# Kernel tuning notes

Hardware: AMD Instinct MI355X
Metric: run time of the kernel (lower is better)

The kernel has to match this reference:

```python
import jax, jax.numpy as jnp
import numpy as np

B, N, F, D, H, L, K = 128, 128, 13, 256, 8, 8, 10
FF = 2 * D  # FFN / hidden width
HEAD = D // H


def setup_inputs() -> dict:
    key = jax.random.key(0)
    ks = iter(jax.random.split(key, 64))
    def nrm(shape, scale=0.02):
        return jax.random.normal(next(ks), shape, dtype=jnp.float32) * scale
    return {
        "input_features": jax.random.normal(next(ks), (B, N, F), dtype=jnp.float32),
        "input_points": jax.random.normal(next(ks), (B, N, 2), dtype=jnp.float32),
        "input_mask": jnp.ones((B, N, 1), dtype=jnp.float32),
        "input_time": jax.random.uniform(next(ks), (B, 1), dtype=jnp.float32),
        # get_encoding: Dense(2D, gelu) -> Dense(D, gelu)
        "enc_w1": nrm((F, FF)), "enc_b1": jnp.zeros((FF,), jnp.float32),
        "enc_w2": nrm((FF, D)), "enc_b2": jnp.zeros((D,), jnp.float32),
        # FourierProjection MLP (no bias, swish)
        "four_w1": nrm((D, FF)), "four_w2": nrm((FF, D)),
        # FiLM time projection (no bias)
        "time_w": nrm((D, FF)),
        # local KNN MLPs: round 0 input 2*F, round 1 input 2*D
        "loc1_w1": nrm((2 * F, FF)), "loc1_b1": jnp.zeros((FF,), jnp.float32),
        "loc1_w2": nrm((FF, D)), "loc1_b2": jnp.zeros((D,), jnp.float32),
        "loc2_w1": nrm((2 * D, FF)), "loc2_b1": jnp.zeros((FF,), jnp.float32),
        "loc2_w2": nrm((FF, D)), "loc2_b2": jnp.zeros((D,), jnp.float32),
        # transformer encoder layers, stacked over L
        "qkv_w": nrm((L, D, 3 * D)), "qkv_b": jnp.zeros((L, 3 * D), jnp.float32),
        "out_w": nrm((L, D, D)), "out_b": jnp.zeros((L, D), jnp.float32),
        "ln1_g": jnp.ones((L, D), jnp.float32), "ln1_b": jnp.zeros((L, D), jnp.float32),
        "ff1_w": nrm((L, D, FF)), "ff1_b": jnp.zeros((L, FF), jnp.float32),
        "ff2_w": nrm((L, FF, D)), "ff2_b": jnp.zeros((L, D), jnp.float32),
        "gamma": jnp.full((L, D), 1e-5, dtype=jnp.float32),
        "ln2_g": jnp.ones((L, D), jnp.float32), "ln2_b": jnp.zeros((L, D), jnp.float32),
    }


def _ln(x, g, b, eps=1e-5):
    m = jnp.mean(x, axis=-1, keepdims=True)
    v = jnp.var(x, axis=-1, keepdims=True)
    return (x - m) * jax.lax.rsqrt(v + eps) * g + b


def _fourier(t, w1, w2):
    # t: (B,1) -> (B,D)
    half = D // 2
    emb = np.log(10000.0) / (half - 1)
    freq = jnp.exp(-emb * jnp.arange(half, dtype=jnp.float32))
    angle = t * freq[None, :] * 1000.0  # (B, half)
    e = jnp.concatenate([jnp.sin(angle), jnp.cos(angle)], axis=-1)
    e = jax.nn.silu(e @ w1)
    return jax.nn.silu(e @ w2)


def _get_neighbors(points, feats, w1, b1, w2, b2):
    # points: (B,N,P), feats: (B,N,C) -> (B,N,D)
    r = jnp.sum(points * points, axis=-1)  # (B,N)
    d = r[:, :, None] - 2.0 * jnp.einsum('bnp,bmp->bnm', points, points) + r[:, None, :]
    _, idx = jax.lax.top_k(-d, K + 1)
    idx = idx[:, :, 1:]  # drop self, (B,N,K)
    knn = jax.vmap(lambda f, i: f[i])(feats, idx)  # (B,N,K,C)
    center = jnp.broadcast_to(feats[:, :, None, :], knn.shape)
    local = jnp.concatenate([knn - center, center], axis=-1)  # (B,N,K,2C)
    local = jax.nn.gelu(local @ w1 + b1)
    local = jax.nn.gelu(local @ w2 + b2)
    return jnp.mean(local, axis=2)


def _mha(x, mask, wqkv, bqkv, wo, bo):
    Bx, Nx, _ = x.shape
    qkv = x @ wqkv + bqkv
    q, k, v = jnp.split(qkv, 3, axis=-1)
    def heads(t):
        return t.reshape(Bx, Nx, H, HEAD).transpose(0, 2, 1, 3)
    q, k, v = heads(q), heads(k), heads(v)
    scores = jnp.einsum('bhqd,bhkd->bhqk', q, k) * (1.0 / np.sqrt(HEAD))
    keep = mask[:, None, None, :, 0] > 0  # (B,1,1,N)
    scores = jnp.where(keep, scores, -1e9)
    a = jax.nn.softmax(scores, axis=-1)
    o = jnp.einsum('bhqk,bhkd->bhqd', a, v).transpose(0, 2, 1, 3).reshape(Bx, Nx, D)
    return o @ wo + bo


def _pet(input_features, input_points, input_mask, input_time,
         enc_w1, enc_b1, enc_w2, enc_b2, four_w1, four_w2, time_w,
         loc1_w1, loc1_b1, loc1_w2, loc1_b2, loc2_w1, loc2_b1, loc2_w2, loc2_b2,
         qkv_w, qkv_b, out_w, out_b, ln1_g, ln1_b, ff1_w, ff1_b, ff2_w, ff2_b,
         gamma, ln2_g, ln2_b):
    # feature encoding (RandomDrop is identity at eval / feature_drop=0)
    enc = jax.nn.gelu(input_features @ enc_w1 + enc_b1)
    enc = jax.nn.gelu(enc @ enc_w2 + enc_b2)  # (B,N,D)
    # FiLM time conditioning
    t = _fourier(input_time, four_w1, four_w2)  # (B,D)
    t = t[:, None, :] * input_mask  # (B,N,D)
    scale, shift = jnp.split(t @ time_w, 2, axis=-1)
    enc = enc * (1.0 + scale) + shift
    # local KNN aggregation
    coord_shift = 999.0 * (1.0 - input_mask)  # (B,N,1)
    points = input_points[:, :, :2]
    lf = _get_neighbors(coord_shift + points, input_features, loc1_w1, loc1_b1, loc1_w2, loc1_b2)
    lf = _get_neighbors(coord_shift + lf, lf, loc2_w1, loc2_b1, loc2_w2, loc2_b2)
    enc = enc + lf
    skip = enc
    x = enc
    for i in range(L):
        res = x
        a = _mha(x, input_mask, qkv_w[i], qkv_b[i], out_w[i], out_b[i])
        x = _ln(res + a, ln1_g[i], ln1_b[i])
        res = x
        h = jax.nn.gelu(x @ ff1_w[i] + ff1_b[i])
        h = h @ ff2_w[i] + ff2_b[i]
        h = h * gamma[i] * input_mask  # LayerScale with mask
        x = _ln(res + h, ln2_g[i], ln2_b[i])
    return x + skip


def reference(input_features, input_points, input_mask, input_time,
              enc_w1, enc_b1, enc_w2, enc_b2, four_w1, four_w2, time_w,
              loc1_w1, loc1_b1, loc1_w2, loc1_b2, loc2_w1, loc2_b1, loc2_w2, loc2_b2,
              qkv_w, qkv_b, out_w, out_b, ln1_g, ln1_b, ff1_w, ff1_b, ff2_w, ff2_b,
              gamma, ln2_g, ln2_b):
    return _pet(input_features, input_points, input_mask, input_time,
                enc_w1, enc_b1, enc_w2, enc_b2, four_w1, four_w2, time_w,
                loc1_w1, loc1_b1, loc1_w2, loc1_b2, loc2_w1, loc2_b1, loc2_w2, loc2_b2,
                qkv_w, qkv_b, out_w, out_b, ln1_g, ln1_b, ff1_w, ff1_b, ff2_w, ff2_b,
                gamma, ln2_g, ln2_b)
```

## Files before the change

### kernel.cpp

```cpp
#include <hip/hip_runtime.h>
#include <hip/hip_bf16.h>
#include <cmath>

#define DEV_INLINE __device__ __forceinline__

constexpr int Bn = 128;
constexpr int Nn = 128;
constexpr int Fn = 13;
constexpr int Dn = 256;
constexpr int Ln = 8;
constexpr int Kn = 10;
constexpr int FFn = 512;
constexpr int Tn = Bn * Nn;
constexpr int Rn = Tn * Kn;

typedef __attribute__((ext_vector_type(4))) float f32x4;
typedef __attribute__((ext_vector_type(8))) short bf16x8;
typedef unsigned short us;

__device__ float g_x[Tn * Dn];
__device__ float g_skip[Tn * Dn];
__device__ float g_big[Tn * Dn];
__device__ float g_dm[Tn * Nn];
__device__ float g_u[Bn * FFn];
__device__ float g_r[Tn];
__device__ float g_pqbias[2048];
__device__ int   g_idx[Rn];
__device__ us g_bigb[Tn * 768];
__device__ us g_xb[Tn * Dn];
__device__ us g_attb[Tn * Dn];
__device__ us g_lf1b[Tn * Dn];
__device__ us g_pq[Tn * 1024];
__device__ us g_h2b[Rn * Dn];
__device__ us g_feat16[Tn * 32];
constexpr int OFF_ENC1 = 0;
constexpr int OFF_ENC2 = OFF_ENC1 + 512 * 32;
constexpr int OFF_W2A  = OFF_ENC2 + 256 * 512;
constexpr int OFF_W2B  = OFF_W2A + 256 * 512;
constexpr int OFF_PQ1  = OFF_W2B + 256 * 512;
constexpr int OFF_PQ2  = OFF_PQ1 + 1024 * 32;
constexpr int OFF_QKV  = OFF_PQ2 + 1024 * 256;
constexpr int OFF_OUT  = OFF_QKV + 8 * 768 * 256;
constexpr int OFF_FF1  = OFF_OUT + 8 * 256 * 256;
constexpr int OFF_FF2  = OFF_FF1 + 8 * 512 * 256;
constexpr int WT_TOTAL = OFF_FF2 + 8 * 256 * 512;
__device__ us g_wt[WT_TOTAL];

DEV_INLINE float gelu_f(float x) {
    float x2 = x * x;
    float m = x * fmaf(x2, -0.07135537f, -1.59576912f);
    float t = __expf(m);
    return x * __builtin_amdgcn_rcpf(1.f + t);
}
DEV_INLINE us f2b(float x) {
    __hip_bfloat16 h = __float2bfloat16(x);
    return *(us*)&h;
}
DEV_INLINE float blo(unsigned u) { return __uint_as_float(u << 16); }
DEV_INLINE float bhi(unsigned u) { return __uint_as_float(u & 0xFFFF0000u); }
DEV_INLINE unsigned pk2(float a, float b) {
    float2 f; f.x = a; f.y = b;
    __hip_bfloat162 h = __float22bfloat162_rn(f);
    return *(unsigned*)&h;
}

#define GLOAD16(gp, lp)                                                            \
    __builtin_amdgcn_global_load_lds(                                              \
        (const __attribute__((address_space(1))) unsigned int*)(gp),               \
        (__attribute__((address_space(3))) unsigned int*)(lp), 16, 0, 0)

constexpr int U0 = 0;
constexpr int U1 = U0 + 2;
constexpr int U2 = U1 + 16;
constexpr int U3 = U2 + 16;
constexpr int U4 = U3 + 16;
constexpr int U5 = U4 + 192;
constexpr int U6 = U5 + 64;
constexpr int U7 = U6 + 128;
constexpr int U8 = U7 + 128;
constexpr int U9 = U8 + 128;
constexpr int U10 = U9 + 128;
constexpr int U11 = U10 + 256;
constexpr int U12 = U11 + 128;
constexpr int UPN = U12 + 128;

DEV_INLINE void prep_seg(const float* __restrict__ src, us* __restrict__ dst,
                         int Kreal, int Kpad, int Nd, long sstride, long dstride,
                         int gx, int gy, int lb, int tid, float* tile) {
    int z = lb / (gx * gy);
    int rem = lb - z * gx * gy;
    int by = rem / gx, bx = rem - by * gx;
    const float* s = src + (size_t)z * sstride;
    us* d = dst + (size_t)z * dstride;
    int cn = tid & 31, rk = tid >> 5;
    int kbase = by * 32, nbase = bx * 32;
#pragma unroll
    for (int p = 0; p < 4; p++) {
        int k = kbase + p * 8 + rk;
        float v = (k < Kreal) ? s[(size_t)k * Nd + nbase + cn] : 0.f;
        tile[(p * 8 + rk) * 33 + cn] = v;
    }
    __syncthreads();
#pragma unroll
    for (int p = 0; p < 4; p++) {
        int nl = p * 8 + rk;
        d[(size_t)(nbase + nl) * Kpad + kbase + cn] = f2b(tile[cn * 33 + nl]);
    }
    __syncthreads();
}

DEV_INLINE void prepPQ_seg(const float* __restrict__ w1, const float* __restrict__ b1,
                           us* __restrict__ dst, float* __restrict__ bdst,
                           int Kreal, int Kpad, int n, int tid) {
    for (int k = tid; k < Kpad; k += 256) {
        float v;
        if (n < 512) v = (k < Kreal) ? w1[(size_t)k * 512 + n] : 0.f;
        else {
            int m = n - 512;
            v = (k < Kreal) ? (w1[(size_t)(Kreal + k) * 512 + m] - w1[(size_t)k * 512 + m]) : 0.f;
        }
        dst[(size_t)n * Kpad + k] = f2b(v);
    }
    if (tid == 0) bdst[n] = (n < 512) ? 0.f : b1[n - 512];
}

__global__ __launch_bounds__(256) void k_uprep(
    const float* __restrict__ enc_w1, const float* __restrict__ enc_w2,
    const float* __restrict__ l1w2, const float* __restrict__ l2w2,
    const float* __restrict__ qkv_w, const float* __restrict__ out_w,
    const float* __restrict__ ff1w, const float* __restrict__ ff2w,
    const float* __restrict__ l1w1, const float* __restrict__ l1b1,
    const float* __restrict__ l2w1, const float* __restrict__ l2b1,
    const float* __restrict__ feat, const float* __restrict__ tin,
    const float* __restrict__ four_w1, const float* __restrict__ four_w2,
    const float* __restrict__ time_w, const float* __restrict__ pts,
    const float* __restrict__ mask,
    us* __restrict__ wt, float* __restrict__ pqbias, us* __restrict__ fp,
    float* __restrict__ u, int* __restrict__ idx) {
    __shared__ float shmem[1056];
    int b = blockIdx.x, tid = threadIdx.x;
    if (b < U1) {
#pragma unroll 1
        for (int i = 0; i < 8; i++)
            prep_seg(enc_w1, wt + OFF_ENC1, 13, 32, 512, 0, 0, 16, 1, (b - U0) * 8 + i, tid, shmem);
    } else if (b < U2) {
#pragma unroll 1
        for (int i = 0; i < 8; i++)
            prep_seg(enc_w2, wt + OFF_ENC2, 512, 512, 256, 0, 0, 8, 16, (b - U1) * 8 + i, tid, shmem);
    } else if (b < U3) {
#pragma unroll 1
        for (int i = 0; i < 8; i++)
            prep_seg(l1w2, wt + OFF_W2A, 512, 512, 256, 0, 0, 8, 16, (b - U2) * 8 + i, tid, shmem);
    } else if (b < U4) {
#pragma unroll 1
        for (int i = 0; i < 8; i++)
            prep_seg(l2w2, wt + OFF_W2B, 512, 512, 256, 0, 0, 8, 16, (b - U3) * 8 + i, tid, shmem);
    } else if (b < U5) {
#pragma unroll 1
        for (int i = 0; i < 8; i++)
            prep_seg(qkv_w, wt + OFF_QKV, 256, 256, 768, 256 * 768, 768 * 256, 24, 8, (b - U4) * 8 + i, tid, shmem);
    } else if (b < U6) {
#pragma unroll 1
        for (int i = 0; i < 8; i++)
            prep_seg(out_w, wt + OFF_OUT, 256, 256, 256, 256 * 256, 256 * 256, 8, 8, (b - U5) * 8 + i, tid, shmem);
    } else if (b < U7) {
#pragma unroll 1
        for (int i = 0; i < 8; i++)
            prep_seg(ff1w, wt + OFF_FF1, 256, 256, 512, 256 * 512, 512 * 256, 16, 8, (b - U6) * 8 + i, tid, shmem);
    } else if (b < U8) {
#pragma unroll 1
        for (int i = 0; i < 8; i++)
            prep_seg(ff2w, wt + OFF_FF2, 512, 512, 256, 512 * 256, 256 * 512, 8, 16, (b - U7) * 8 + i, tid, shmem);
    } else if (b < U9) {
#pragma unroll 1
        for (int i = 0; i < 8; i++)
            prepPQ_seg(l1w1, l1b1, wt + OFF_PQ1, pqbias, 13, 32, (b - U8) * 8 + i, tid);
    } else if (b < U10) {
#pragma unroll 1
        for (int i = 0; i < 8; i++)
            prepPQ_seg(l2w1, l2b1, wt + OFF_PQ2, pqbias + 1024, 256, 256, (b - U9) * 8 + i, tid);
    } else if (b < U11) {
#pragma unroll 1
        for (int i = 0; i < 8; i++) {
            int gid = ((b - U10) * 8 + i) * 256 + tid;
            int t = gid >> 5, c = gid & 31;
            fp[gid] = (c < Fn) ? f2b(feat[(size_t)t * Fn + c]) : (us)0;
        }
    } else if (b < U12) {
        float* e = shmem; float* e1 = shmem + 256; float* t2 = shmem + 768;
        int bb = b - U11;
        float tv = tin[bb];
        if (tid < 128) {
            const float emb = 0.07252236513366287f;
            float fr = expf(-emb * (float)tid);
            float ang = tv * fr * 1000.f;
            e[tid] = sinf(ang);
            e[tid + 128] = cosf(ang);
        }
        __syncthreads();
        for (int j = tid; j < 512; j += 256) {
            float s = 0.f;
            for (int i = 0; i < 256; i++) s += e[i] * four_w1[(size_t)i * 512 + j];
            e1[j] = s / (1.f + expf(-s));
        }
        __syncthreads();
        {
            float s = 0.f;
            for (int i = 0; i < 512; i++) s += e1[i] * four_w2[(size_t)i * 256 + tid];
            t2[tid] = s / (1.f + expf(-s));
        }
        __syncthreads();
        for (int j = tid; j < 512; j += 256) {
            float s = 0.f;
            for (int i = 0; i < 256; i++) s += t2[i] * time_w[(size_t)i * 512 + j];
            u[(size_t)bb * 512 + j] = s;
        }
    } else {
        float* px = shmem; float* py = shmem + 128; float* rr = shmem + 256;
        int bb = b - U12;
        if (tid < 128) {
            int n = tid;
            float shift = 999.f * (1.f - mask[bb * Nn + n]);
            float x = pts[(size_t)(bb * Nn + n) * 2 + 0] + shift;
            float y = pts[(size_t)(bb * Nn + n) * 2 + 1] + shift;
            px[n] = x; py[n] = y; rr[n] = x * x + y * y;
        }
        __syncthreads();
        if (tid < 128) {
            int n = tid;
            float x = px[n], y = py[n], rn = rr[n];
            float bd[Kn + 1]; int bi[Kn + 1];
#pragma unroll
            for (int j = 0; j <= Kn; j++) { bd[j] = 3.4e38f; bi[j] = -1; }
            for (int m = 0; m < Nn; m++) {
                float d = rn - 2.f * (x * px[m] + y * py[m]) + rr[m];
                if (d < bd[Kn]) {
                    int j = Kn;
                    while (j > 0 && d < bd[j - 1]) { bd[j] = bd[j - 1]; bi[j] = bi[j - 1]; j--; }
                    bd[j] = d; bi[j] = m;
                }
            }
            for (int j = 1; j <= Kn; j++) idx[(size_t)(bb * Nn + n) * Kn + j - 1] = bi[j];
        }
    }
}

template <int EPI, bool OBF>
__global__ __launch_bounds__(256) void k_mg2(const us* __restrict__ A,
                                             const us* __restrict__ Bt,
                                             const float* __restrict__ bias,
                                             void* __restrict__ Cp,
                                             int Kd, int Nd) {
    __shared__ __align__(16) us As[128 * 32];
    __shared__ __align__(16) us Bs[128 * 32];
    int tid = threadIdx.x;
    int m0 = blockIdx.y << 7, n0 = blockIdx.x << 7;
    int wave = tid >> 6, lane = tid & 63;
    int wm = (wave & 1) << 6, wn = (wave >> 1) << 6;
    int lm = lane & 15, quad = lane >> 4;
    int r0 = (wave << 5) + (lane >> 2);
    int colu = (((lane & 3) ^ ((lane >> 2) & 3)) << 3);
    const us* pa0 = A + (size_t)(m0 + r0) * Kd + colu;
    const us* pa1 = A + (size_t)(m0 + r0 + 16) * Kd + colu;
    const us* pb0 = Bt + (size_t)(n0 + r0) * Kd + colu;
    const us* pb1 = Bt + (size_t)(n0 + r0 + 16) * Kd + colu;
    auto lAs = (__attribute__((address_space(3))) us*)As;
    auto lBs = (__attribute__((address_space(3))) us*)Bs;
    int lbase = wave << 10;
    int fcol = ((quad ^ (lm & 3)) << 3);
    f32x4 acc[4][4] = {};
    for (int k0 = 0; k0 < Kd; k0 += 32) {
        __syncthreads();
        GLOAD16(pa0 + k0, lAs + lbase);
        GLOAD16(pa1 + k0, lAs + lbase + 512);
        GLOAD16(pb0 + k0, lBs + lbase);
        GLOAD16(pb1 + k0, lBs + lbase + 512);
        __syncthreads();
        bf16x8 afr[4], bfr[4];
#pragma unroll
        for (int i = 0; i < 4; i++) {
            afr[i] = *(const bf16x8*)&As[(wm + i * 16 + lm) * 32 + fcol];
            bfr[i] = *(const bf16x8*)&Bs[(wn + i * 16 + lm) * 32 + fcol];
        }
#pragma unroll
        for (int mf = 0; mf < 4; mf++)
#pragma unroll
            for (int nf = 0; nf < 4; nf++)
                acc[mf][nf] = __builtin_amdgcn_mfma_f32_16x16x32_bf16(afr[mf], bfr[nf], acc[mf][nf], 0, 0, 0);
    }
    float bvs[4];
#pragma unroll
    for (int nf = 0; nf < 4; nf++) bvs[nf] = bias[n0 + wn + nf * 16 + lm];
#pragma unroll
    for (int mf = 0; mf < 4; mf++) {
#pragma unroll
        for (int r = 0; r < 4; r++) {
            size_t row = (size_t)(m0 + wm + mf * 16 + (quad << 2) + r);
#pragma unroll
            for (int nf = 0; nf < 4; nf++) {
                float v = acc[mf][nf][r] + bvs[nf];
                if (EPI == 1) v = gelu_f(v);
                size_t ci = row * Nd + n0 + wn + nf * 16 + lm;
                if constexpr (OBF) ((us*)Cp)[ci] = f2b(v);
                else ((float*)Cp)[ci] = v;
            }
        }
    }
}

__global__ __launch_bounds__(256) void k_qattn(const us* __restrict__ xb,
                                               const us* __restrict__ Bt,
                                               const float* __restrict__ bias,
                                               const float* __restrict__ mask,
                                               us* __restrict__ attb) {
    __shared__ __align__(16) char smem[64512];
    us* Ps = (us*)smem;
    us* Qs = (us*)(smem + 34816);
    us* Ks = (us*)(smem + 45056);
    us* Vt = (us*)(smem + 55296);
    float* msk = (float*)(smem + 64000);
    us* As = (us*)smem;
    us* Bs = (us*)(smem + 8192);
    int bh = blockIdx.x;
    int b = bh >> 3, h = bh & 7;
    int tid = threadIdx.x;
    int wave = tid >> 6, lane = tid & 63;
    int lm = lane & 15, quad = lane >> 4;
    int wm = wave << 5;
    int colu = (((lane & 3) ^ ((lane >> 2) & 3)) << 3);
    int r0 = (wave << 5) + (lane >> 2);
    const us* pa0 = xb + (size_t)(b * 128 + r0) * 256 + colu;
    const us* pa1 = xb + (size_t)(b * 128 + r0 + 16) * 256 + colu;
    int seg0 = wave, seg1 = wave + 4;
    int n0_ = seg0 * 16 + (lane >> 2);
    int n1_ = seg1 * 16 + (lane >> 2);
    int g0 = (n0_ >> 5) * 256 + h * 32 + (n0_ & 31);
    int g1 = (n1_ >> 5) * 256 + h * 32 + (n1_ & 31);
    const us* pb0 = Bt + (size_t)g0 * 256 + colu;
    const us* pb1 = Bt + (size_t)g1 * 256 + colu;
    auto lAs = (__attribute__((address_space(3))) us*)As;
    auto lBs = (__attribute__((address_space(3))) us*)Bs;
    int fcol = ((quad ^ (lm & 3)) << 3);
    f32x4 gacc[2][6] = {};
    for (int k0 = 0; k0 < 256; k0 += 32) {
        __syncthreads();
        GLOAD16(pa0 + k0, lAs + (wave << 10));
        GLOAD16(pa1 + k0, lAs + (wave << 10) + 512);
        GLOAD16(pb0 + k0, lBs + (seg0 << 9));
        if (wave < 2) GLOAD16(pb1 + k0, lBs + (seg1 << 9));
        __syncthreads();
        bf16x8 afr[2], bfr[6];
#pragma unroll
        for (int mf = 0; mf < 2; mf++)
            afr[mf] = *(const bf16x8*)&As[(wm + mf * 16 + lm) * 32 + fcol];
#pragma unroll
        for (int nf = 0; nf < 6; nf++)
            bfr[nf] = *(const bf16x8*)&Bs[(nf * 16 + lm) * 32 + fcol];
#pragma unroll
        for (int mf = 0; mf < 2; mf++)
#pragma unroll
            for (int nf = 0; nf < 6; nf++)
                gacc[mf][nf] = __builtin_amdgcn_mfma_f32_16x16x32_bf16(afr[mf], bfr[nf], gacc[mf][nf], 0, 0, 0);
    }
    float bvq[6];
#pragma unroll
    for (int nf = 0; nf < 6; nf++) {
        int n = nf * 16 + lm;
        bvq[nf] = bias[(n >> 5) * 256 + h * 32 + (n & 31)];
    }
    __syncthreads();
#pragma unroll
    for (int mf = 0; mf < 2; mf++) {
#pragma unroll
        for (int r = 0; r < 4; r++) {
            int row = wm + mf * 16 + (quad << 2) + r;
#pragma unroll
            for (int nf = 0; nf < 6; nf++) {
                us hv = f2b(gacc[mf][nf][r] + bvq[nf]);
                int n = nf * 16 + lm;
                if (nf < 2) Qs[row * 40 + n] = hv;
                else if (nf < 4) Ks[row * 40 + (n - 32)] = hv;
                else Vt[(n - 64) * 136 + row] = hv;
            }
        }
    }
    if (tid < 128) msk[tid] = mask[b * 128 + tid];
    __syncthreads();
    f32x4 acc[2][8] = {};
    {
        bf16x8 aq[2];
#pragma unroll
        for (int mf = 0; mf < 2; mf++)
            aq[mf] = *(const bf16x8*)&Qs[(wm + mf * 16 + lm) * 40 + (quad << 3)];
#pragma unroll
        for (int nf = 0; nf < 8; nf++) {
            bf16x8 bk = *(const bf16x8*)&Ks[(nf * 16 + lm) * 40 + (quad << 3)];
            acc[0][nf] = __builtin_amdgcn_mfma_f32_16x16x32_bf16(aq[0], bk, acc[0][nf], 0, 0, 0);
            acc[1][nf] = __builtin_amdgcn_mfma_f32_16x16x32_bf16(aq[1], bk, acc[1][nf], 0, 0, 0);
        }
    }
    {
        const float sc = 0.17677669529663687f;
        float mkc[8];
#pragma unroll
        for (int nf = 0; nf < 8; nf++) mkc[nf] = msk[nf * 16 + lm];
#pragma unroll
        for (int mf = 0; mf < 2; mf++) {
#pragma unroll
            for (int nf = 0; nf < 8; nf++)
#pragma unroll
                for (int r = 0; r < 4; r++) {
                    float s = acc[mf][nf][r];
                    acc[mf][nf][r] = mkc[nf] > 0.f ? s * sc : -1.0e9f;
                }
#pragma unroll
            for (int r = 0; r < 4; r++) {
                float m = acc[mf][0][r];
#pragma unroll
                for (int nf = 1; nf < 8; nf++) m = fmaxf(m, acc[mf][nf][r]);
                m = fmaxf(m, __shfl_xor(m, 1, 64));
                m = fmaxf(m, __shfl_xor(m, 2, 64));
                m = fmaxf(m, __shfl_xor(m, 4, 64));
                m = fmaxf(m, __shfl_xor(m, 8, 64));
                float s = 0.f;
#pragma unroll
                for (int nf = 0; nf < 8; nf++) {
                    float p = __expf(acc[mf][nf][r] - m);
                    acc[mf][nf][r] = p;
                    s += p;
                }
                s += __shfl_xor(s, 1, 64);
                s += __shfl_xor(s, 2, 64);
                s += __shfl_xor(s, 4, 64);
                s += __shfl_xor(s, 8, 64);
                float linv = __builtin_amdgcn_rcpf(s);
                int prow = wm + mf * 16 + (quad << 2) + r;
#pragma unroll
                for (int nf = 0; nf < 8; nf++)
                    Ps[prow * 136 + nf * 16 + lm] = f2b(acc[mf][nf][r] * linv);
            }
        }
    }
    __syncthreads();
    f32x4 oacc[2][2] = {};
    for (int kt = 0; kt < 4; kt++) {
        bf16x8 ap[2], bv[2];
#pragma unroll
        for (int mf = 0; mf < 2; mf++)
            ap[mf] = *(const bf16x8*)&Ps[(wm + mf * 16 + lm) * 136 + kt * 32 + (quad << 3)];
#pragma unroll
        for (int nf = 0; nf < 2; nf++)
            bv[nf] = *(const bf16x8*)&Vt[(nf * 16 + lm) * 136 + kt * 32 + (quad << 3)];
#pragma unroll
        for (int mf = 0; mf < 2; mf++)
#pragma unroll
            for (int nf = 0; nf < 2; nf++)
                oacc[mf][nf] = __builtin_amdgcn_mfma_f32_16x16x32_bf16(ap[mf], bv[nf], oacc[mf][nf], 0, 0, 0);
    }
#pragma unroll
    for (int mf = 0; mf < 2; mf++)
#pragma unroll
        for (int r = 0; r < 4; r++) {
            int row = wm + mf * 16 + (quad << 2) + r;
#pragma unroll
            for (int nf = 0; nf < 2; nf++)
                attb[(size_t)(b * 128 + row) * 256 + h * 32 + nf * 16 + lm] = f2b(oacc[mf][nf][r]);
        }
}

template <bool PM, bool FINAL>
__global__ __launch_bounds__(512) void k_mgln(const us* __restrict__ A,
                                              const us* __restrict__ Bt,
                                              const float* __restrict__ bias,
                                              const us* __restrict__ res,
                                              const float* __restrict__ gamma,
                                              const float* __restrict__ mask,
                                              const float* __restrict__ lng,
                                              const float* __restrict__ lnb,
                                              const float* __restrict__ skip,
                                              us* __restrict__ xbout,
                                              float* __restrict__ finout,
                                              int Kd) {
    __shared__ __align__(16) us As[64 * 32];
    __shared__ __align__(16) us Bs[256 * 32];
    __shared__ float2 part[8][64];
    __shared__ float2 stat[64];
    int tid = threadIdx.x;
    int m0 = blockIdx.x << 6;
    int wave = tid >> 6, lane = tid & 63;
    int wn = wave << 5;
    int lm = lane & 15, quad = lane >> 4;
    int colu = (((lane & 3) ^ ((lane >> 2) & 3)) << 3);
    int ar = (wave << 4) + (lane >> 2);
    int br = (wave << 5) + (lane >> 2);
    const us* pa = A + (size_t)(m0 + ar) * Kd + colu;
    const us* pb0 = Bt + (size_t)br * Kd + colu;
    const us* pb1 = Bt + (size_t)(br + 16) * Kd + colu;
    auto lAs = (__attribute__((address_space(3))) us*)As;
    auto lBs = (__attribute__((address_space(3))) us*)Bs;
    int fcol = ((quad ^ (lm & 3)) << 3);
    f32x4 acc[4][2] = {};
    for (int k0 = 0; k0 < Kd; k0 += 32) {
        __syncthreads();
        if (wave < 4) GLOAD16(pa + k0, lAs + (wave << 9));
        GLOAD16(pb0 + k0, lBs + (wave << 10));
        GLOAD16(pb1 + k0, lBs + (wave << 10) + 512);
        __syncthreads();
        bf16x8 afr[4], bfr[2];
#pragma unroll
        for (int i = 0; i < 4; i++)
            afr[i] = *(const bf16x8*)&As[(i * 16 + lm) * 32 + fcol];
#pragma unroll
        for (int j = 0; j < 2; j++)
            bfr[j] = *(const bf16x8*)&Bs[(wn + j * 16 + lm) * 32 + fcol];
#pragma unroll
        for (int mf = 0; mf < 4; mf++)
#pragma unroll
            for (int nf = 0; nf < 2; nf++)
                acc[mf][nf] = __builtin_amdgcn_mfma_f32_16x16x32_bf16(afr[mf], bfr[nf], acc[mf][nf], 0, 0, 0);
    }
    float bvs[2], gms[2];
#pragma unroll
    for (int nf = 0; nf < 2; nf++) {
        int col = wn + nf * 16 + lm;
        bvs[nf] = bias[col];
        if (PM) gms[nf] = gamma[col];
    }
#pragma unroll
    for (int mf = 0; mf < 4; mf++) {
#pragma unroll
        for (int r = 0; r < 4; r++) {
            int rowl = mf * 16 + (quad << 2) + r;
            size_t row = (size_t)(m0 + rowl);
            float mrow = PM ? mask[row] : 0.f;
            float s1 = 0.f, s2 = 0.f;
#pragma unroll
            for (int nf = 0; nf < 2; nf++) {
                int col = wn + nf * 16 + lm;
                float rv = blo((unsigned)res[row * 256 + col]);
                float v = acc[mf][nf][r] + bvs[nf];
                v = PM ? fmaf(v * gms[nf], mrow, rv) : rv + v;
                acc[mf][nf][r] = v;
                s1 += v; s2 += v * v;
            }
            s1 += __shfl_xor(s1, 1, 64); s2 += __shfl_xor(s2, 1, 64);
            s1 += __shfl_xor(s1, 2, 64); s2 += __shfl_xor(s2, 2, 64);
            s1 += __shfl_xor(s1, 4, 64); s2 += __shfl_xor(s2, 4, 64);
            s1 += __shfl_xor(s1, 8, 64); s2 += __shfl_xor(s2, 8, 64);
            if (lm == 0) { float2 p; p.x = s1; p.y = s2; part[wave][rowl] = p; }
        }
    }
    __syncthreads();
    if (tid < 64) {
        float s = 0.f, q = 0.f;
#pragma unroll
        for (int w = 0; w < 8; w++) { float2 p = part[w][tid]; s += p.x; q += p.y; }
        float mean = s * (1.f / 256.f);
        float var = q * (1.f / 256.f) - mean * mean;
        float2 st; st.x = mean; st.y = rsqrtf(var + 1e-5f);
        stat[tid] = st;
    }
    __syncthreads();
    float gvs[2], bts[2];
#pragma unroll
    for (int nf = 0; nf < 2; nf++) {
        int col = wn + nf * 16 + lm;
        gvs[nf] = lng[col];
        bts[nf] = lnb[col];
    }
#pragma unroll
    for (int mf = 0; mf < 4; mf++) {
#pragma unroll
        for (int r = 0; r < 4; r++) {
            int rowl = mf * 16 + (quad << 2) + r;
            size_t row = (size_t)(m0 + rowl);
            float2 st = stat[rowl];
#pragma unroll
            for (int nf = 0; nf < 2; nf++) {
                int col = wn + nf * 16 + lm;
                float nv = fmaf((acc[mf][nf][r] - st.x) * st.y, gvs[nf], bts[nf]);
                if (FINAL) finout[row * 256 + col] = nv + skip[row * 256 + col];
                else xbout[row * 256 + col] = f2b(nv);
            }
        }
    }
}

__global__ __launch_bounds__(512) void k_knng(const us* __restrict__ pq,
                                              const int* __restrict__ idx,
                                              const us* __restrict__ Bt,
                                              const float* __restrict__ bias,
                                              us* __restrict__ h2b) {
    __shared__ __align__(16) us As[128 * 64];
    __shared__ __align__(16) us Bs[256 * 64];
    int tid = threadIdx.x;
    int m0 = blockIdx.x << 7;
    int wave = tid >> 6, lane = tid & 63;
    int wm = (wave & 1) << 6, wn = (wave >> 1) << 6;
    int lm = lane & 15, quad = lane >> 4;
    int arow = tid >> 2, acolu = (tid & 3) << 4;
    int asw = arow & 7;
    int ablk0 = ((tid & 3) << 1) ^ asw, ablk1 = (((tid & 3) << 1) + 1) ^ asw;
    int r = m0 + arow;
    int tok = r / 10;
    int nb = idx[r];
    int prow = (tok & ~127) + nb;
    const us* Pp = pq + (size_t)prow * 1024 + acolu;
    const us* Qp = pq + (size_t)tok * 1024 + 512 + acolu;
    int brow = (wave << 5) + (lane >> 3);
    int bcol = (((lane & 7) ^ (lane >> 3)) << 3);
    const us* pb = Bt + (size_t)brow * 512 + bcol;
    auto lBs = (__attribute__((address_space(3))) us*)Bs;
    int lbase = wave << 11;
    int fsw = lm & 7;
    f32x4 acc[4][4] = {};
    for (int k0 = 0; k0 < 512; k0 += 64) {
        uint4 pv0 = *(const uint4*)(Pp + k0);
        uint4 pv1 = *(const uint4*)(Pp + k0 + 8);
        uint4 qv0 = *(const uint4*)(Qp + k0);
        uint4 qv1 = *(const uint4*)(Qp + k0 + 8);
        uint4 h0, h1;
        h0.x = pk2(gelu_f(blo(pv0.x) + blo(qv0.x)), gelu_f(bhi(pv0.x) + bhi(qv0.x)));
        h0.y = pk2(gelu_f(blo(pv0.y) + blo(qv0.y)), gelu_f(bhi(pv0.y) + bhi(qv0.y)));
        h0.z = pk2(gelu_f(blo(pv0.z) + blo(qv0.z)), gelu_f(bhi(pv0.z) + bhi(qv0.z)));
        h0.w = pk2(gelu_f(blo(pv0.w) + blo(qv0.w)), gelu_f(bhi(pv0.w) + bhi(qv0.w)));
        h1.x = pk2(gelu_f(blo(pv1.x) + blo(qv1.x)), gelu_f(bhi(pv1.x) + bhi(qv1.x)));
        h1.y = pk2(gelu_f(blo(pv1.y) + blo(qv1.y)), gelu_f(bhi(pv1.y) + bhi(qv1.y)));
        h1.z = pk2(gelu_f(blo(pv1.z) + blo(qv1.z)), gelu_f(bhi(pv1.z) + bhi(qv1.z)));
        h1.w = pk2(gelu_f(blo(pv1.w) + blo(qv1.w)), gelu_f(bhi(pv1.w) + bhi(qv1.w)));
        __syncthreads();
        GLOAD16(pb + k0, lBs + lbase);
        GLOAD16(pb + k0 + 8 * 512, lBs + lbase + 512);
        GLOAD16(pb + k0 + 16 * 512, lBs + lbase + 1024);
        GLOAD16(pb + k0 + 24 * 512, lBs + lbase + 1536);
        *(uint4*)&As[arow * 64 + (ablk0 << 3)] = h0;
        *(uint4*)&As[arow * 64 + (ablk1 << 3)] = h1;
        __syncthreads();
#pragma unroll
        for (int sub = 0; sub < 2; sub++) {
            int lblk = (sub << 2) + quad;
            int fcol = ((lblk ^ fsw) << 3);
            bf16x8 afr[4], bfr[4];
#pragma unroll
            for (int i = 0; i < 4; i++) {
                afr[i] = *(const bf16x8*)&As[(wm + i * 16 + lm) * 64 + fcol];
                bfr[i] = *(const bf16x8*)&Bs[(wn + i * 16 + lm) * 64 + fcol];
            }
#pragma unroll
            for (int mf = 0; mf < 4; mf++)
#pragma unroll
                for (int nf = 0; nf < 4; nf++)
                    acc[mf][nf] = __builtin_amdgcn_mfma_f32_16x16x32_bf16(afr[mf], bfr[nf], acc[mf][nf], 0, 0, 0);
        }
    }
    float bvs[4];
#pragma unroll
    for (int nf = 0; nf < 4; nf++) bvs[nf] = bias[wn + nf * 16 + lm];
#pragma unroll
    for (int mf = 0; mf < 4; mf++) {
#pragma unroll
        for (int rr = 0; rr < 4; rr++) {
            size_t row = (size_t)(m0 + wm + mf * 16 + (quad << 2) + rr);
#pragma unroll
            for (int nf = 0; nf < 4; nf++) {
                float v = gelu_f(acc[mf][nf][rr] + bvs[nf]);
                h2b[row * 256 + wn + nf * 16 + lm] = f2b(v);
            }
        }
    }
}

__global__ __launch_bounds__(64) void k_mean1s(const us* __restrict__ h2b,
                                               const float* __restrict__ mask,
                                               us* __restrict__ lfb,
                                               float* __restrict__ big,
                                               float* __restrict__ r) {
    int t = blockIdx.x, lane = threadIdx.x;
    int c = lane << 2;
    const us* p = h2b + (size_t)t * Kn * 256 + c;
    float s0 = 0.f, s1 = 0.f, s2 = 0.f, s3 = 0.f;
#pragma unroll
    for (int k = 0; k < Kn; k++) {
        uint2 v = *(const uint2*)(p + k * 256);
        s0 += blo(v.x); s1 += bhi(v.x);
        s2 += blo(v.y); s3 += bhi(v.y);
    }
    s0 *= 0.1f; s1 *= 0.1f; s2 *= 0.1f; s3 *= 0.1f;
    uint2 ob; ob.x = pk2(s0, s1); ob.y = pk2(s2, s3);
    *(uint2*)&lfb[(size_t)t * 256 + c] = ob;
    float sh = 999.f * (1.f - mask[t]);
    float4 w; w.x = s0 + sh; w.y = s1 + sh; w.z = s2 + sh; w.w = s3 + sh;
    *(float4*)&big[(size_t)t * 256 + c] = w;
    float sq = w.x * w.x + w.y * w.y + w.z * w.z + w.w * w.w;
#pragma unroll
    for (int off = 32; off; off >>= 1) sq += __shfl_xor(sq, off, 64);
    if (lane == 0) r[t] = sq;
}

__global__ __launch_bounds__(256) void k_dist(const float* __restrict__ fe,
                                              const float* __restrict__ r,
                                              float* __restrict__ Dm) {
    int b = blockIdx.z;
    int m0 = blockIdx.x * 64, n0 = blockIdx.y * 64;
    const float* A = fe + (size_t)b * Nn * Dn;
    __shared__ float As[16][68];
    __shared__ float Bs[16][68];
    int tid = threadIdx.x;
    int tx = tid & 15, ty = tid >> 4;
    int ar = tid >> 2, ac = (tid & 3) << 2;
    float acc[4][4] = {};
    for (int k0 = 0; k0 < Dn; k0 += 16) {
        float4 av = *(const float4*)&A[(size_t)(n0 + ar) * Dn + k0 + ac];
        float4 bv = *(const float4*)&A[(size_t)(m0 + ar) * Dn + k0 + ac];
        __syncthreads();
        As[ac + 0][ar] = av.x; As[ac + 1][ar] = av.y; As[ac + 2][ar] = av.z; As[ac + 3][ar] = av.w;
        Bs[ac + 0][ar] = bv.x; Bs[ac + 1][ar] = bv.y; Bs[ac + 2][ar] = bv.z; Bs[ac + 3][ar] = bv.w;
        __syncthreads();
#pragma unroll
        for (int kk = 0; kk < 16; kk++) {
            float4 a = *(const float4*)&As[kk][ty << 2];
            float4 b2 = *(const float4*)&Bs[kk][tx << 2];
            acc[0][0] += a.x * b2.x; acc[0][1] += a.x * b2.y; acc[0][2] += a.x * b2.z; acc[0][3] += a.x * b2.w;
            acc[1][0] += a.y * b2.x; acc[1][1] += a.y * b2.y; acc[1][2] += a.y * b2.z; acc[1][3] += a.y * b2.w;
            acc[2][0] += a.z * b2.x; acc[2][1] += a.z * b2.y; acc[2][2] += a.z * b2.z; acc[2][3] += a.z * b2.w;
            acc[3][0] += a.w * b2.x; acc[3][1] += a.w * b2.y; acc[3][2] += a.w * b2.z; acc[3][3] += a.w * b2.w;
        }
    }
    float4 rm = *(const float4*)&r[b * Nn + m0 + (tx << 2)];
#pragma unroll
    for (int i = 0; i < 4; i++) {
        int n = n0 + (ty << 2) + i;
        float rn = r[b * Nn + n];
        float4 v;
        v.x = rn - 2.f * acc[i][0] + rm.x;
        v.y = rn - 2.f * acc[i][1] + rm.y;
        v.z = rn - 2.f * acc[i][2] + rm.z;
        v.w = rn - 2.f * acc[i][3] + rm.w;
        *(float4*)&Dm[(size_t)b * Nn * Nn + (size_t)n * Nn + m0 + (tx << 2)] = v;
    }
}

__global__ __launch_bounds__(128) void k_topkg(const float* __restrict__ Dm, int* __restrict__ idx) {
    int b = blockIdx.x, n = threadIdx.x;
    const float* row = Dm + (size_t)b * Nn * Nn + (size_t)n * Nn;
    float bd[Kn + 1]; int bi[Kn + 1];
#pragma unroll
    for (int j = 0; j <= Kn; j++) { bd[j] = 3.4e38f; bi[j] = -1; }
    for (int m = 0; m < Nn; m++) {
        float d = row[m];
        if (d < bd[Kn]) {
            int j = Kn;
            while (j > 0 && d < bd[j - 1]) { bd[j] = bd[j - 1]; bi[j] = bi[j - 1]; j--; }
            bd[j] = d; bi[j] = m;
        }
    }
    for (int j = 1; j <= Kn; j++) idx[(size_t)(b * Nn + n) * Kn + j - 1] = bi[j];
}

__global__ __launch_bounds__(256) void k_meanc(const us* __restrict__ h2b,
                                               const float* __restrict__ u,
                                               const float* __restrict__ mask,
                                               const float* __restrict__ x,
                                               float* __restrict__ skip,
                                               us* __restrict__ xb) {
    int t = blockIdx.x, c = threadIdx.x;
    const us* p = h2b + (size_t)t * Kn * 256 + c;
    float s = 0.f;
#pragma unroll
    for (int k = 0; k < Kn; k++) s += blo((unsigned)p[k * 256]);
    s *= 0.1f;
    int b = t >> 7;
    float m = mask[t];
    float xv = x[(size_t)t * Dn + c];
    float sc = u[(size_t)b * 512 + c];
    float sh = u[(size_t)b * 512 + 256 + c];
    float v = xv * (1.f + m * sc) + m * sh + s;
    skip[(size_t)t * Dn + c] = v;
    xb[(size_t)t * Dn + c] = f2b(v);
}

extern "C" void kernel_launch(void* const* d_in, const int* in_sizes, int n_in,
                              void* d_out, int out_size, void* d_ws, size_t ws_size,
                              hipStream_t stream) {
    (void)in_sizes; (void)n_in; (void)out_size; (void)d_ws; (void)ws_size;
    const float* f_feat = (const float*)d_in[0];
    const float* f_pts  = (const float*)d_in[1];
    const float* f_mask = (const float*)d_in[2];
    const float* f_time = (const float*)d_in[3];
    const float* enc_w1 = (const float*)d_in[4];
    const float* enc_b1 = (const float*)d_in[5];
    const float* enc_w2 = (const float*)d_in[6];
    const float* enc_b2 = (const float*)d_in[7];
    const float* four_w1 = (const float*)d_in[8];
    const float* four_w2 = (const float*)d_in[9];
    const float* time_w = (const float*)d_in[10];
    const float* l1w1 = (const float*)d_in[11];
    const float* l1b1 = (const float*)d_in[12];
    const float* l1w2 = (const float*)d_in[13];
    const float* l1b2 = (const float*)d_in[14];
    const float* l2w1 = (const float*)d_in[15];
    const float* l2b1 = (const float*)d_in[16];
    const float* l2w2 = (const float*)d_in[17];
    const float* l2b2 = (const float*)d_in[18];
    const float* qkv_w = (const float*)d_in[19];
    const float* qkv_b = (const float*)d_in[20];
    const float* out_w = (const float*)d_in[21];
    const float* out_b = (const float*)d_in[22];
    const float* ln1g = (const float*)d_in[23];
    const float* ln1b = (const float*)d_in[24];
    const float* ff1w = (const float*)d_in[25];
    const float* ff1b = (const float*)d_in[26];
    const float* ff2w = (const float*)d_in[27];
    const float* ff2b = (const float*)d_in[28];
    const float* gam  = (const float*)d_in[29];
    const float* ln2g = (const float*)d_in[30];
    const float* ln2b = (const float*)d_in[31];
    float* out = (float*)d_out;

    float *x, *skip, *big, *dm, *u, *r, *pqbias;
    int* idx;
    us *bigb, *xb, *attb, *lf1b, *pq, *h2b, *feat16, *wt;
    hipGetSymbolAddress((void**)&x,    HIP_SYMBOL(g_x));
    hipGetSymbolAddress((void**)&skip, HIP_SYMBOL(g_skip));
    hipGetSymbolAddress((void**)&big,  HIP_SYMBOL(g_big));
    hipGetSymbolAddress((void**)&dm,   HIP_SYMBOL(g_dm));
    hipGetSymbolAddress((void**)&u,    HIP_SYMBOL(g_u));
    hipGetSymbolAddress((void**)&r,    HIP_SYMBOL(g_r));
    hipGetSymbolAddress((void**)&pqbias, HIP_SYMBOL(g_pqbias));
    hipGetSymbolAddress((void**)&idx,  HIP_SYMBOL(g_idx));
    hipGetSymbolAddress((void**)&bigb, HIP_SYMBOL(g_bigb));
    hipGetSymbolAddress((void**)&xb,   HIP_SYMBOL(g_xb));
    hipGetSymbolAddress((void**)&attb, HIP_SYMBOL(g_attb));
    hipGetSymbolAddress((void**)&lf1b, HIP_SYMBOL(g_lf1b));
    hipGetSymbolAddress((void**)&pq,   HIP_SYMBOL(g_pq));
    hipGetSymbolAddress((void**)&h2b,  HIP_SYMBOL(g_h2b));
    hipGetSymbolAddress((void**)&feat16, HIP_SYMBOL(g_feat16));
    hipGetSymbolAddress((void**)&wt,   HIP_SYMBOL(g_wt));

    k_uprep<<<UPN, 256, 0, stream>>>(
        enc_w1, enc_w2, l1w2, l2w2, qkv_w, out_w, ff1w, ff2w,
        l1w1, l1b1, l2w1, l2b1, f_feat, f_time, four_w1, four_w2, time_w,
        f_pts, f_mask, wt, pqbias, feat16, u, idx);

    k_mg2<1, true><<<dim3(4, 128), 256, 0, stream>>>(feat16, wt + OFF_ENC1, enc_b1, bigb, 32, 512);
    k_mg2<1, false><<<dim3(2, 128), 256, 0, stream>>>(bigb, wt + OFF_ENC2, enc_b2, x, 512, 256);
    k_mg2<0, true><<<dim3(8, 128), 256, 0, stream>>>(feat16, wt + OFF_PQ1, pqbias, pq, 32, 1024);
    k_knng<<<Rn / 128, 512, 0, stream>>>(pq, idx, wt + OFF_W2A, l1b2, h2b);
    k_mean1s<<<Tn, 64, 0, stream>>>(h2b, f_mask, lf1b, big, r);
    k_dist<<<dim3(2, 2, Bn), 256, 0, stream>>>(big, r, dm);
    k_topkg<<<Bn, Nn, 0, stream>>>(dm, idx);
    k_mg2<0, true><<<dim3(8, 128), 256, 0, stream>>>(lf1b, wt + OFF_PQ2, pqbias + 1024, pq, 256, 1024);
    k_knng<<<Rn / 128, 512, 0, stream>>>(pq, idx, wt + OFF_W2B, l2b2, h2b);
    k_meanc<<<Tn, 256, 0, stream>>>(h2b, u, f_mask, x, skip, xb);
    for (int l = 0; l < Ln; l++) {
        k_qattn<<<Bn * 8, 256, 0, stream>>>(
            xb, wt + OFF_QKV + (size_t)l * 768 * 256, qkv_b + l * 768, f_mask, attb);
        k_mgln<false, false><<<256, 512, 0, stream>>>(
            attb, wt + OFF_OUT + (size_t)l * 256 * 256, out_b + l * 256,
            xb, nullptr, f_mask, ln1g + l * Dn, ln1b + l * Dn, nullptr, xb, nullptr, 256);
        k_mg2<1, true><<<dim3(4, 128), 256, 0, stream>>>(
            xb, wt + OFF_FF1 + (size_t)l * 512 * 256, ff1b + l * 512, bigb, 256, 512);
        if (l < Ln - 1)
            k_mgln<true, false><<<256, 512, 0, stream>>>(
                bigb, wt + OFF_FF2 + (size_t)l * 256 * 512, ff2b + l * 256,
                xb, gam + l * Dn, f_mask, ln2g + l * Dn, ln2b + l * Dn, nullptr, xb, nullptr, 512);
        else
            k_mgln<true, true><<<256, 512, 0, stream>>>(
                bigb, wt + OFF_FF2 + (size_t)l * 256 * 512, ff2b + l * 256,
                xb, gam + l * Dn, f_mask, ln2g + l * Dn, ln2b + l * Dn, skip, nullptr, out, 512);
    }
}
```

Measured before the change: 1.342 ms.

## Fuse out-projection+LayerNorm with FF1 GEMM+GELU in one kernel

Adds a fused kernel that runs the attention output projection, residual add and LayerNorm for a 64-row tile, keeps the normalized bf16 rows in swizzled shared memory, and then computes the FF1 GEMM with bias and GELU from that tile. This replaces the separate k_mgln and k_mg2 launches in each transformer layer, saving one launch and the global re-read of the normalized activations. The cost is lower FF1 parallelism, since 256 blocks now each do the full 512-column FF1 sequentially in two halves instead of a 4x128 grid. Shared memory use also grows to about 57KB, which may reduce occupancy.

```diff
diff --git a/kernel.cpp b/kernel.cpp
--- a/kernel.cpp
+++ b/kernel.cpp
@@ -466,6 +466,165 @@
             for (int nf = 0; nf < 2; nf++)
                 attb[(size_t)(b * 128 + row) * 256 + h * 32 + nf * 16 + lm] = f2b(oacc[mf][nf][r]);
         }
+}
+
+__global__ __launch_bounds__(512) void k_mglnff(const us* __restrict__ A,
+                                                const us* __restrict__ Bt,
+                                                const float* __restrict__ bias,
+                                                const us* __restrict__ res,
+                                                const float* __restrict__ lng,
+                                                const float* __restrict__ lnb,
+                                                const us* __restrict__ W1t,
+                                                const float* __restrict__ b1,
+                                                us* __restrict__ xbout,
+                                                us* __restrict__ ffout) {
+    __shared__ __align__(16) char smem[57856];
+    us* xln = (us*)smem;
+    us* As = (us*)(smem + 32768);
+    us* Bs = (us*)(smem + 36864);
+    us* Bs2 = (us*)(smem + 32768);
+    float2* part = (float2*)(smem + 53248);
+    float2* stat = (float2*)(smem + 57344);
+    int tid = threadIdx.x;
+    int m0 = blockIdx.x << 6;
+    int wave = tid >> 6, lane = tid & 63;
+    int wn = wave << 5;
+    int lm = lane & 15, quad = lane >> 4;
+    int colu = (((lane & 3) ^ ((lane >> 2) & 3)) << 3);
+    int ar = (wave << 4) + (lane >> 2);
+    int br = (wave << 5) + (lane >> 2);
+    const us* pa = A + (size_t)(m0 + ar) * 256 + colu;
+    const us* pb0 = Bt + (size_t)br * 256 + colu;
+    const us* pb1 = Bt + (size_t)(br + 16) * 256 + colu;
+    auto lAs = (__attribute__((address_space(3))) us*)As;
+    auto lBs = (__attribute__((address_space(3))) us*)Bs;
+    auto lBs2 = (__attribute__((address_space(3))) us*)Bs2;
+    int fcol = ((quad ^ (lm & 3)) << 3);
+    f32x4 acc[4][2] = {};
+    for (int k0 = 0; k0 < 256; k0 += 32) {
+        __syncthreads();
+        if (wave < 4) GLOAD16(pa + k0, lAs + (wave << 9));
+        GLOAD16(pb0 + k0, lBs + (wave << 10));
+        GLOAD16(pb1 + k0, lBs + (wave << 10) + 512);
+        __syncthreads();
+        bf16x8 afr[4], bfr[2];
+#pragma unroll
+        for (int i = 0; i < 4; i++)
+            afr[i] = *(const bf16x8*)&As[(i * 16 + lm) * 32 + fcol];
+#pragma unroll
+        for (int j = 0; j < 2; j++)
+            bfr[j] = *(const bf16x8*)&Bs[(wn + j * 16 + lm) * 32 + fcol];
+#pragma unroll
+        for (int mf = 0; mf < 4; mf++)
+#pragma unroll
+            for (int nf = 0; nf < 2; nf++)
+                acc[mf][nf] = __builtin_amdgcn_mfma_f32_16x16x32_bf16(afr[mf], bfr[nf], acc[mf][nf], 0, 0, 0);
+    }
+    float bvs[2];
+#pragma unroll
+    for (int nf = 0; nf < 2; nf++) bvs[nf] = bias[wn + nf * 16 + lm];
+#pragma unroll
+    for (int mf = 0; mf < 4; mf++) {
+#pragma unroll
+        for (int r = 0; r < 4; r++) {
+            int rowl = mf * 16 + (quad << 2) + r;
+            size_t row = (size_t)(m0 + rowl);
+            float s1 = 0.f, s2 = 0.f;
+#pragma unroll
+            for (int nf = 0; nf < 2; nf++) {
+                int col = wn + nf * 16 + lm;
+                float rv = blo((unsigned)res[row * 256 + col]);
+                float v = rv + acc[mf][nf][r] + bvs[nf];
+                acc[mf][nf][r] = v;
+                s1 += v; s2 += v * v;
+            }
+            s1 += __shfl_xor(s1, 1, 64); s2 += __shfl_xor(s2, 1, 64);
+            s1 += __shfl_xor(s1, 2, 64); s2 += __shfl_xor(s2, 2, 64);
+            s1 += __shfl_xor(s1, 4, 64); s2 += __shfl_xor(s2, 4, 64);
+            s1 += __shfl_xor(s1, 8, 64); s2 += __shfl_xor(s2, 8, 64);
+            if (lm == 0) { float2 p; p.x = s1; p.y = s2; part[wave * 64 + rowl] = p; }
+        }
+    }
+    __syncthreads();
+    if (tid < 64) {
+        float s = 0.f, q = 0.f;
+#pragma unroll
+        for (int w = 0; w < 8; w++) { float2 p = part[w * 64 + tid]; s += p.x; q += p.y; }
+        float mean = s * (1.f / 256.f);
+        float var = q * (1.f / 256.f) - mean * mean;
+        float2 st; st.x = mean; st.y = rsqrtf(var + 1e-5f);
+        stat[tid] = st;
+    }
+    __syncthreads();
+    float gvs[2], bts[2];
+#pragma unroll
+    for (int nf = 0; nf < 2; nf++) {
+        int col = wn + nf * 16 + lm;
+        gvs[nf] = lng[col];
+        bts[nf] = lnb[col];
+    }
+#pragma unroll
+    for (int mf = 0; mf < 4; mf++) {
+#pragma unroll
+        for (int r = 0; r < 4; r++) {
+            int rowl = mf * 16 + (quad << 2) + r;
+            size_t row = (size_t)(m0 + rowl);
+            float2 st = stat[rowl];
+#pragma unroll
+            for (int nf = 0; nf < 2; nf++) {
+                int col = wn + nf * 16 + lm;
+                float nv = fmaf((acc[mf][nf][r] - st.x) * st.y, gvs[nf], bts[nf]);
+                us hv = f2b(nv);
+                xbout[row * 256 + col] = hv;
+                int phys = (col >> 3) ^ (rowl & 31);
+                xln[rowl * 256 + (phys << 3) + (col & 7)] = hv;
+            }
+        }
+    }
+#pragma unroll 1
+    for (int nh = 0; nh < 2; nh++) {
+        const us* Bt2 = W1t + (size_t)(nh * 256) * 256;
+        const us* qb0 = Bt2 + (size_t)br * 256 + colu;
+        const us* qb1 = Bt2 + (size_t)(br + 16) * 256 + colu;
+        f32x4 acc2[4][2] = {};
+        for (int k0 = 0; k0 < 256; k0 += 32) {
+            __syncthreads();
+            GLOAD16(qb0 + k0, lBs2 + (wave << 10));
+            GLOAD16(qb1 + k0, lBs2 + (wave << 10) + 512);
+            __syncthreads();
+            bf16x8 afr[4], bfr[2];
+#pragma unroll
+            for (int i = 0; i < 4; i++) {
+                int rowi = i * 16 + lm;
+                int lblk = (k0 >> 3) + quad;
+                int phys = lblk ^ (rowi & 31);
+                afr[i] = *(const bf16x8*)&xln[rowi * 256 + (phys << 3)];
+            }
+#pragma unroll
+            for (int j = 0; j < 2; j++)
+                bfr[j] = *(const bf16x8*)&Bs2[(wn + j * 16 + lm) * 32 + fcol];
+#pragma unroll
+            for (int mf = 0; mf < 4; mf++)
+#pragma unroll
+                for (int nf = 0; nf < 2; nf++)
+                    acc2[mf][nf] = __builtin_amdgcn_mfma_f32_16x16x32_bf16(afr[mf], bfr[nf], acc2[mf][nf], 0, 0, 0);
+        }
+        float b2v[2];
+#pragma unroll
+        for (int nf = 0; nf < 2; nf++) b2v[nf] = b1[nh * 256 + wn + nf * 16 + lm];
+#pragma unroll
+        for (int mf = 0; mf < 4; mf++) {
+#pragma unroll
+            for (int r = 0; r < 4; r++) {
+                size_t row = (size_t)(m0 + mf * 16 + (quad << 2) + r);
+#pragma unroll
+                for (int nf = 0; nf < 2; nf++) {
+                    float v = gelu_f(acc2[mf][nf][r] + b2v[nf]);
+                    ffout[row * 512 + nh * 256 + wn + nf * 16 + lm] = f2b(v);
+                }
+            }
+        }
+    }
 }
 
 template <bool PM, bool FINAL>
@@ -855,11 +1014,10 @@
     for (int l = 0; l < Ln; l++) {
         k_qattn<<<Bn * 8, 256, 0, stream>>>(
             xb, wt + OFF_QKV + (size_t)l * 768 * 256, qkv_b + l * 768, f_mask, attb);
-        k_mgln<false, false><<<256, 512, 0, stream>>>(
+        k_mglnff<<<256, 512, 0, stream>>>(
             attb, wt + OFF_OUT + (size_t)l * 256 * 256, out_b + l * 256,
-            xb, nullptr, f_mask, ln1g + l * Dn, ln1b + l * Dn, nullptr, xb, nullptr, 256);
-        k_mg2<1, true><<<dim3(4, 128), 256, 0, stream>>>(
-            xb, wt + OFF_FF1 + (size_t)l * 512 * 256, ff1b + l * 512, bigb, 256, 512);
+            xb, ln1g + l * Dn, ln1b + l * Dn,
+            wt + OFF_FF1 + (size_t)l * 512 * 256, ff1b + l * 512, xb, bigb);
         if (l < Ln - 1)
             k_mgln<true, false><<<256, 512, 0, stream>>>(
                 bigb, wt + OFF_FF2 + (size_t)l * 256 * 512, ff2b + l * 256,
```

After: 1.301 ms, median of 2. 1.03x faster.
